# Optimization experiments

Measured on AMD Instinct MI355X. Metric: run time of the kernel, lower is better.

The kernel has to match this reference:

```python
import jax, jax.numpy as jnp
import numpy as np

EPS = 1e-5  # torch InstanceNorm1d default eps


def _instance_norm(x, gamma, beta):
    # per-sample, per-channel stats over the length dim; biased variance (torch semantics)
    mu = jnp.mean(x, axis=-1, keepdims=True)
    var = jnp.var(x, axis=-1, keepdims=True)
    return (x - mu) / jnp.sqrt(var + EPS) * gamma[None, :, None] + beta[None, :, None]


def _forward(x_ft, gamma, beta):
    # x_ft: complex [B, C, N]
    N = x_ft.shape[-1]
    x = jnp.real(jnp.fft.ifft(x_ft, norm='forward'))  # [B, C, N] real
    # The torch loop runs res = base_res .. N, each iteration overwriting the
    # low/high frequency bands of x_out in-place. The final iteration
    # (res == N) writes EVERY entry of x_out (the two band slices cover all
    # N//2+1 rfft bins), so the module's output -- and its gradients, since
    # overwritten writes carry zero cotangent -- equal the res == N
    # computation alone. resample_1d(x, N) copies the full spectrum and is a
    # spectral identity, so x_res == x.
    xr = _instance_norm(x, gamma, beta)
    xr = jax.nn.gelu(xr, approximate=False)  # exact GELU, matches torch nn.GELU
    # Faithful to the source: inside the loop torch.fft.rfft2 is used, i.e. a
    # 2D transform over the last two dims (channel, length).
    x_out = jnp.fft.rfft2(xr, norm='forward')  # complex [B, C, N//2 + 1]
    out = jnp.fft.fft(jnp.fft.irfft(x_out, n=N, norm='forward'), norm='forward')
    return out  # complex [B, C, N]


def setup_inputs() -> dict:
    key = jax.random.key(0)
    k1, k2 = jax.random.split(key)
    B, C, N = 16, 128, 8192
    return {
        'x_ft_real': jax.random.normal(k1, (B, C, N), dtype=jnp.float32),
        'x_ft_imag': jax.random.normal(k2, (B, C, N), dtype=jnp.float32),
        'gamma': jnp.ones((C,), dtype=jnp.float32),
        'beta': jnp.zeros((C,), dtype=jnp.float32),
    }


def reference(x_ft_real, x_ft_imag, gamma, beta):
    out = _forward(jax.lax.complex(x_ft_real, x_ft_imag), gamma, beta)
    # return real/imag parts as separate float arrays (harness-friendly)
    return (jnp.real(out), jnp.imag(out))
```

## Files before the change

kernel.cpp:

```cpp
#include <hip/hip_runtime.h>
#include <math.h>

static constexpr int kN = 8192;
static constexpr int kC = 128;
static constexpr int kB = 16;
static constexpr float kScale = 0.5f / 1048576.0f;

#define C8  0.70710678118654752f
#define CP8 0.92387953251128676f
#define SP8 0.38268343236508977f

typedef float v2f __attribute__((ext_vector_type(2)));

__device__ __forceinline__ v2f mk2(float x, float y){ v2f r; r.x=x; r.y=y; return r; }
__device__ __forceinline__ v2f imul(v2f a){ return mk2(-a.y, a.x); }
__device__ __forceinline__ v2f mimul(v2f a){ return mk2(a.y, -a.x); }
__device__ __forceinline__ v2f cconj(v2f a){ return mk2(a.x, -a.y); }
__device__ __forceinline__ v2f cmul(v2f a, v2f b){
    return mk2(a.x*b.x - a.y*b.y, a.x*b.y + a.y*b.x);
}

__device__ __forceinline__ v2f wrev(float rev){
    return mk2(__builtin_amdgcn_cosf(rev), __builtin_amdgcn_sinf(rev));
}

__device__ __forceinline__ int swz(int n){ return n ^ ((n>>4)&15); }

#define REV(k) ((((k)&3)<<2)|((k)>>2))

template<int SGN>
__device__ __forceinline__ void dft4(v2f&a, v2f&b, v2f&c, v2f&d){
    v2f t0=a+c, t1=a-c, t2=b+d, t3=b-d;
    v2f j3 = (SGN>0) ? imul(t3) : mimul(t3);
    a = t0+t2; b = t1+j3; c = t0-t2; d = t1-j3;
}

template<int SGN>
__device__ __forceinline__ void dft16(v2f* v){
    dft4<SGN>(v[0], v[4], v[8],  v[12]);
    dft4<SGN>(v[1], v[5], v[9],  v[13]);
    dft4<SGN>(v[2], v[6], v[10], v[14]);
    dft4<SGN>(v[3], v[7], v[11], v[15]);
    const float sg = (SGN>0)? 1.f : -1.f;
    const v2f W1 = mk2(CP8,  sg*SP8);
    const v2f W2 = mk2(C8,   sg*C8);
    const v2f W3 = mk2(SP8,  sg*CP8);
    const v2f W6 = mk2(-C8,  sg*C8);
    const v2f W9 = mk2(-CP8, -sg*SP8);
    v[5]  = cmul(v[5],  W1);
    v[9]  = cmul(v[9],  W2);
    v[13] = cmul(v[13], W3);
    v[6]  = cmul(v[6],  W2);
    v[10] = (SGN>0)? imul(v[10]) : mimul(v[10]);
    v[14] = cmul(v[14], W6);
    v[7]  = cmul(v[7],  W3);
    v[11] = cmul(v[11], W6);
    v[15] = cmul(v[15], W9);
    dft4<SGN>(v[0],  v[1],  v[2],  v[3]);
    dft4<SGN>(v[4],  v[5],  v[6],  v[7]);
    dft4<SGN>(v[8],  v[9],  v[10], v[11]);
    dft4<SGN>(v[12], v[13], v[14], v[15]);
}

__device__ __forceinline__ void twid_dif(v2f* v, v2f w1){
    v2f w2=cmul(w1,w1), w3=cmul(w2,w1), w4=cmul(w2,w2);
    v2f w5=cmul(w2,w3), w6=cmul(w3,w3), w7=cmul(w3,w4), w8=cmul(w4,w4);
    v2f w9=cmul(w4,w5), w10=cmul(w5,w5), w11=cmul(w5,w6), w12=cmul(w6,w6);
    v2f w13=cmul(w6,w7), w14=cmul(w7,w7), w15=cmul(w7,w8);
    v[4] =cmul(v[4], w1);  v[8] =cmul(v[8], w2);  v[12]=cmul(v[12],w3);
    v[1] =cmul(v[1], w4);  v[5] =cmul(v[5], w5);  v[9] =cmul(v[9], w6);
    v[13]=cmul(v[13],w7);  v[2] =cmul(v[2], w8);  v[6] =cmul(v[6], w9);
    v[10]=cmul(v[10],w10); v[14]=cmul(v[14],w11); v[3] =cmul(v[3], w12);
    v[7] =cmul(v[7], w13); v[11]=cmul(v[11],w14); v[15]=cmul(v[15],w15);
}
__device__ __forceinline__ void twid_dit(v2f* v, v2f w1){
    v2f w2=cmul(w1,w1), w3=cmul(w2,w1), w4=cmul(w2,w2);
    v2f w5=cmul(w2,w3), w6=cmul(w3,w3), w7=cmul(w3,w4), w8=cmul(w4,w4);
    v2f w9=cmul(w4,w5), w10=cmul(w5,w5), w11=cmul(w5,w6), w12=cmul(w6,w6);
    v2f w13=cmul(w6,w7), w14=cmul(w7,w7), w15=cmul(w7,w8);
    v[1] =cmul(v[1], w1);  v[2] =cmul(v[2], w2);  v[3] =cmul(v[3], w3);
    v[4] =cmul(v[4], w4);  v[5] =cmul(v[5], w5);  v[6] =cmul(v[6], w6);
    v[7] =cmul(v[7], w7);  v[8] =cmul(v[8], w8);  v[9] =cmul(v[9], w9);
    v[10]=cmul(v[10],w10); v[11]=cmul(v[11],w11); v[12]=cmul(v[12],w12);
    v[13]=cmul(v[13],w13); v[14]=cmul(v[14],w14); v[15]=cmul(v[15],w15);
}

__device__ __forceinline__ v2f gelu2(v2f v){
    v2f z = v * (0.7978845608028654f + 0.0356774081363001f * v * v);
    float e0 = __builtin_amdgcn_exp2f(-2.8853900817779268f * z.x);
    float e1 = __builtin_amdgcn_exp2f(-2.8853900817779268f * z.y);
    return mk2(v.x / (1.0f + e0), v.y / (1.0f + e1));
}

__global__ __launch_bounds__(256, 4) void k1_row(
    const float* __restrict__ xr, const float* __restrict__ xi,
    const float* __restrict__ gamma, const float* __restrict__ beta,
    float* __restrict__ outR, float* __restrict__ outI)
{
    __shared__ v2f buf[4096];
    __shared__ v2f Twb[16];
    __shared__ float sred[4];

    const int p   = threadIdx.x;
    const int row = blockIdx.x;
    const int ch  = row & (kC-1);

    if (p < 16) Twb[p] = wrev((float)p * (1.0f/256.0f));
    const int i0 = ((p>>4)<<8) + (p&15);

    v2f v[16];

    const float* rR = xr + (size_t)row * kN;
    const float* rI = xi + (size_t)row * kN;

    const float mean = 2.0f * rR[0];

    float pq = 0.f;
    #pragma unroll
    for (int j = 0; j < 16; ++j) {
        int k   = p + (j<<8);
        int km  = (kN - k) & (kN-1);
        int km2 = 4096 - k;
        v2f w = wrev((float)k * (1.0f/8192.0f));
        v2f Hk  = mk2(rR[k]+rR[km],       rI[k]-rI[km]);
        v2f Hk2 = mk2(rR[k+4096]+rR[km2], rI[k+4096]-rI[km2]);
        pq += Hk.x*Hk.x + Hk.y*Hk.y + Hk2.x*Hk2.x + Hk2.y*Hk2.y;
        v2f S = Hk + Hk2, D = Hk - Hk2;
        v2f P = cmul(D, w);
        v[j] = S + imul(P);
    }
    #pragma unroll
    for (int off = 32; off >= 1; off >>= 1)
        pq += __shfl_down(pq, off);
    if ((p & 63) == 0) sred[p>>6] = pq;

    dft16<1>(v);
    twid_dif(v, wrev((float)p * (1.0f/4096.0f)));
    #pragma unroll
    for (int m = 0; m < 16; ++m) buf[swz(p + (m<<8))] = v[REV(m)];
    __syncthreads();

    float total = sred[0] + sred[1] + sred[2] + sred[3];
    float var  = total - mean*mean;
    float gg = gamma[ch] * rsqrtf(var + 1e-5f);
    float bb = beta[ch] - mean * gg;

    const v2f wB = Twb[p & 15];
    #pragma unroll
    for (int j = 0; j < 16; ++j) v[j] = buf[swz(i0 + (j<<4))];
    dft16<1>(v);
    twid_dif(v, wB);
    #pragma unroll
    for (int m = 0; m < 16; ++m) buf[swz(i0 + (m<<4))] = v[REV(m)];
    __builtin_amdgcn_wave_barrier();

    #pragma unroll
    for (int j = 0; j < 16; ++j) v[j] = buf[swz((p<<4) + j)];
    dft16<1>(v);

    #pragma unroll
    for (int j = 0; j < 16; ++j) v[j] = gelu2(v[j] * gg + bb);

    {
        v2f u[16];
        #pragma unroll
        for (int j = 0; j < 16; ++j) u[j] = v[REV(j)];
        dft16<-1>(u);
        #pragma unroll
        for (int m = 0; m < 16; ++m) buf[swz((p<<4) + m)] = u[REV(m)];
    }
    __builtin_amdgcn_wave_barrier();

    #pragma unroll
    for (int j = 0; j < 16; ++j) v[j] = buf[swz(i0 + (j<<4))];
    twid_dit(v, cconj(wB));
    dft16<-1>(v);
    #pragma unroll
    for (int m = 0; m < 16; ++m) buf[swz(i0 + (m<<4))] = v[REV(m)];
    __syncthreads();

    #pragma unroll
    for (int j = 0; j < 16; ++j) v[j] = buf[swz(p + (j<<8))];
    twid_dit(v, cconj(wrev((float)p * (1.0f/4096.0f))));
    dft16<-1>(v);
    float* oR = outR + (size_t)row * kN;
    float* oI = outI + (size_t)row * kN;
    #pragma unroll
    for (int m = 0; m < 16; ++m) {
        int k = p + (m<<8);
        oR[k] = v[REV(m)].x;
        oI[k] = v[REV(m)].y;
    }
}

__global__ __launch_bounds__(256, 2) void k2_col(float* __restrict__ outR,
                                                 float* __restrict__ outI)
{
    __shared__ v2f tile[kC][32];
    __shared__ v2f tw[64];

    const int tid  = threadIdx.x;
    const int j    = tid & 31;
    const int g    = tid >> 5;
    const int b    = blockIdx.y;
    const int k0   = blockIdx.x << 5;
    const int colA = k0 + j;
    const bool valid = (colA <= 2048);
    const int colB = (4096 - colA) & 4095;

    if (tid < 64) {
        tw[tid] = mk2(__builtin_amdgcn_cosf((float)tid * (1.0f/128.0f)),
                      -__builtin_amdgcn_sinf((float)tid * (1.0f/128.0f)));
    }
    const float wc =  __builtin_amdgcn_cosf((float)colA * (1.0f/8192.0f));
    const float ws = -__builtin_amdgcn_sinf((float)colA * (1.0f/8192.0f));

    float* baseR = outR + (size_t)b * kC * kN;
    float* baseI = outI + (size_t)b * kC * kN;

    v2f yb[16];
    #pragma unroll
    for (int ci = 0; ci < 16; ++ci) {
        const int c = g + (ci << 3);
        v2f YA = mk2(0.f, 0.f), YB = mk2(0.f, 0.f);
        if (valid) {
            size_t offA = (size_t)c * kN + colA;
            size_t offB = (size_t)c * kN + colB;
            float Zx  = baseR[offA], Zy  = baseI[offA];
            float Zmx = baseR[offB], Zmy = baseI[offB];
            float Sx = Zx + Zmx, Sy = Zy - Zmy;
            float Dx = Zx - Zmx, Dy = Zy + Zmy;
            float Px = Dx*wc - Dy*ws, Py = Dx*ws + Dy*wc;
            YA = mk2(Sx + Py,  Sy - Px);
            YB = mk2(Sx - Py, -Sy - Px);
        }
        tile[c][j] = YA;
        yb[ci] = YB;
    }
    __syncthreads();

    for (int st = 7; st >= 1; --st) {
        const int h = 1 << (st-1);
        #pragma unroll
        for (int s = 0; s < 8; ++s) {
            int q   = g + (s<<3);
            int pos = q & (h-1);
            int i0  = ((q >> (st-1)) << st) + pos;
            int i1  = i0 + h;
            v2f a = tile[i0][j], bb = tile[i1][j];
            v2f w = tw[pos << (7-st)];
            tile[i0][j] = a + bb;
            tile[i1][j] = cmul(a - bb, w);
        }
        __syncthreads();
    }
    if (valid) {
        for (int p = g; p < kC; p += 8) {
            int f = (int)(__brev((unsigned)p) >> 25);
            v2f vv = tile[p][j] * kScale;
            size_t off = (size_t)f * kN + colA;
            if (colA == 0) {
                baseR[off] = vv.x; baseI[off] = 0.f;
            } else {
                baseR[off] = vv.x; baseI[off] = vv.y;
                size_t offm = (size_t)f * kN + (kN - colA);
                baseR[offm] = vv.x; baseI[offm] = -vv.y;
            }
        }
    }
    __syncthreads();

    #pragma unroll
    for (int ci = 0; ci < 16; ++ci) {
        const int c = g + (ci << 3);
        tile[c][j] = yb[ci];
    }
    __syncthreads();

    for (int st = 7; st >= 1; --st) {
        const int h = 1 << (st-1);
        #pragma unroll
        for (int s = 0; s < 8; ++s) {
            int q   = g + (s<<3);
            int pos = q & (h-1);
            int i0  = ((q >> (st-1)) << st) + pos;
            int i1  = i0 + h;
            v2f a = tile[i0][j], bb = tile[i1][j];
            v2f w = tw[pos << (7-st)];
            tile[i0][j] = a + bb;
            tile[i1][j] = cmul(a - bb, w);
        }
        __syncthreads();
    }
    if (valid) {
        const int kkB = 4096 - colA;
        for (int p = g; p < kC; p += 8) {
            int f = (int)(__brev((unsigned)p) >> 25);
            v2f vv = tile[p][j] * kScale;
            size_t off = (size_t)f * kN + kkB;
            if (kkB == 4096) {
                baseR[off] = vv.x; baseI[off] = 0.f;
            } else {
                baseR[off] = vv.x; baseI[off] = vv.y;
                size_t offm = (size_t)f * kN + (kN - kkB);
                baseR[offm] = vv.x; baseI[offm] = -vv.y;
            }
        }
    }
}

extern "C" void kernel_launch(void* const* d_in, const int* in_sizes, int n_in,
                              void* d_out, int out_size, void* d_ws, size_t ws_size,
                              hipStream_t stream)
{
    const float* xr    = (const float*)d_in[0];
    const float* xi    = (const float*)d_in[1];
    const float* gamma = (const float*)d_in[2];
    const float* beta  = (const float*)d_in[3];

    float* outR = (float*)d_out;
    float* outI = outR + (size_t)kB * kC * kN;

    k1_row<<<kB * kC, 256, 0, stream>>>(xr, xi, gamma, beta, outR, outI);
    k2_col<<<dim3(65, kB), 256, 0, stream>>>(outR, outI);
}
```

Before: 107.8 us.

## Process two rows per block in row FFT kernel with float4 LDS packing

The row kernel now handles two rows per 256-thread block, interleaving both rows' FFT stages so twiddle computation, barriers and LDS traffic are shared, with float4 shared-memory accesses carrying both rows. The bit-reverse copy before the inverse DFT16 is replaced by a dft16_rev variant that takes natural-order input. The goal is to amortise per-row fixed costs and raise instruction-level parallelism. In exchange, register pressure roughly doubles, launch bounds drop to 2 blocks per CU, shared memory doubles to 64KB, and the grid halves to 1024 blocks.

After: 117.9 us. +9.4%, slower.

```diff
diff --git a/kernel.cpp b/kernel.cpp
--- a/kernel.cpp
+++ b/kernel.cpp
@@ -62,27 +62,74 @@
     dft4<SGN>(v[12], v[13], v[14], v[15]);
 }
 
-__device__ __forceinline__ void twid_dif(v2f* v, v2f w1){
+template<int SGN>
+__device__ __forceinline__ void dft16_rev(v2f* v){
+    dft4<SGN>(v[0],  v[1],  v[2],  v[3]);
+    dft4<SGN>(v[4],  v[5],  v[6],  v[7]);
+    dft4<SGN>(v[8],  v[9],  v[10], v[11]);
+    dft4<SGN>(v[12], v[13], v[14], v[15]);
+    const float sg = (SGN>0)? 1.f : -1.f;
+    const v2f W1 = mk2(CP8,  sg*SP8);
+    const v2f W2 = mk2(C8,   sg*C8);
+    const v2f W3 = mk2(SP8,  sg*CP8);
+    const v2f W6 = mk2(-C8,  sg*C8);
+    const v2f W9 = mk2(-CP8, -sg*SP8);
+    v[5]  = cmul(v[5],  W1);
+    v[6]  = cmul(v[6],  W2);
+    v[7]  = cmul(v[7],  W3);
+    v[9]  = cmul(v[9],  W2);
+    v[10] = (SGN>0)? imul(v[10]) : mimul(v[10]);
+    v[11] = cmul(v[11], W6);
+    v[13] = cmul(v[13], W3);
+    v[14] = cmul(v[14], W6);
+    v[15] = cmul(v[15], W9);
+    dft4<SGN>(v[0], v[4], v[8],  v[12]);
+    dft4<SGN>(v[1], v[5], v[9],  v[13]);
+    dft4<SGN>(v[2], v[6], v[10], v[14]);
+    dft4<SGN>(v[3], v[7], v[11], v[15]);
+}
+
+__device__ __forceinline__ void twid_dif2(v2f* a, v2f* b, v2f w1){
     v2f w2=cmul(w1,w1), w3=cmul(w2,w1), w4=cmul(w2,w2);
     v2f w5=cmul(w2,w3), w6=cmul(w3,w3), w7=cmul(w3,w4), w8=cmul(w4,w4);
     v2f w9=cmul(w4,w5), w10=cmul(w5,w5), w11=cmul(w5,w6), w12=cmul(w6,w6);
     v2f w13=cmul(w6,w7), w14=cmul(w7,w7), w15=cmul(w7,w8);
-    v[4] =cmul(v[4], w1);  v[8] =cmul(v[8], w2);  v[12]=cmul(v[12],w3);
-    v[1] =cmul(v[1], w4);  v[5] =cmul(v[5], w5);  v[9] =cmul(v[9], w6);
-    v[13]=cmul(v[13],w7);  v[2] =cmul(v[2], w8);  v[6] =cmul(v[6], w9);
-    v[10]=cmul(v[10],w10); v[14]=cmul(v[14],w11); v[3] =cmul(v[3], w12);
-    v[7] =cmul(v[7], w13); v[11]=cmul(v[11],w14); v[15]=cmul(v[15],w15);
-}
-__device__ __forceinline__ void twid_dit(v2f* v, v2f w1){
+    a[4] =cmul(a[4], w1);  b[4] =cmul(b[4], w1);
+    a[8] =cmul(a[8], w2);  b[8] =cmul(b[8], w2);
+    a[12]=cmul(a[12],w3);  b[12]=cmul(b[12],w3);
+    a[1] =cmul(a[1], w4);  b[1] =cmul(b[1], w4);
+    a[5] =cmul(a[5], w5);  b[5] =cmul(b[5], w5);
+    a[9] =cmul(a[9], w6);  b[9] =cmul(b[9], w6);
+    a[13]=cmul(a[13],w7);  b[13]=cmul(b[13],w7);
+    a[2] =cmul(a[2], w8);  b[2] =cmul(b[2], w8);
+    a[6] =cmul(a[6], w9);  b[6] =cmul(b[6], w9);
+    a[10]=cmul(a[10],w10); b[10]=cmul(b[10],w10);
+    a[14]=cmul(a[14],w11); b[14]=cmul(b[14],w11);
+    a[3] =cmul(a[3], w12); b[3] =cmul(b[3], w12);
+    a[7] =cmul(a[7], w13); b[7] =cmul(b[7], w13);
+    a[11]=cmul(a[11],w14); b[11]=cmul(b[11],w14);
+    a[15]=cmul(a[15],w15); b[15]=cmul(b[15],w15);
+}
+__device__ __forceinline__ void twid_dit2(v2f* a, v2f* b, v2f w1){
     v2f w2=cmul(w1,w1), w3=cmul(w2,w1), w4=cmul(w2,w2);
     v2f w5=cmul(w2,w3), w6=cmul(w3,w3), w7=cmul(w3,w4), w8=cmul(w4,w4);
     v2f w9=cmul(w4,w5), w10=cmul(w5,w5), w11=cmul(w5,w6), w12=cmul(w6,w6);
     v2f w13=cmul(w6,w7), w14=cmul(w7,w7), w15=cmul(w7,w8);
-    v[1] =cmul(v[1], w1);  v[2] =cmul(v[2], w2);  v[3] =cmul(v[3], w3);
-    v[4] =cmul(v[4], w4);  v[5] =cmul(v[5], w5);  v[6] =cmul(v[6], w6);
-    v[7] =cmul(v[7], w7);  v[8] =cmul(v[8], w8);  v[9] =cmul(v[9], w9);
-    v[10]=cmul(v[10],w10); v[11]=cmul(v[11],w11); v[12]=cmul(v[12],w12);
-    v[13]=cmul(v[13],w13); v[14]=cmul(v[14],w14); v[15]=cmul(v[15],w15);
+    a[1] =cmul(a[1], w1);  b[1] =cmul(b[1], w1);
+    a[2] =cmul(a[2], w2);  b[2] =cmul(b[2], w2);
+    a[3] =cmul(a[3], w3);  b[3] =cmul(b[3], w3);
+    a[4] =cmul(a[4], w4);  b[4] =cmul(b[4], w4);
+    a[5] =cmul(a[5], w5);  b[5] =cmul(b[5], w5);
+    a[6] =cmul(a[6], w6);  b[6] =cmul(b[6], w6);
+    a[7] =cmul(a[7], w7);  b[7] =cmul(b[7], w7);
+    a[8] =cmul(a[8], w8);  b[8] =cmul(b[8], w8);
+    a[9] =cmul(a[9], w9);  b[9] =cmul(b[9], w9);
+    a[10]=cmul(a[10],w10); b[10]=cmul(b[10],w10);
+    a[11]=cmul(a[11],w11); b[11]=cmul(b[11],w11);
+    a[12]=cmul(a[12],w12); b[12]=cmul(b[12],w12);
+    a[13]=cmul(a[13],w13); b[13]=cmul(b[13],w13);
+    a[14]=cmul(a[14],w14); b[14]=cmul(b[14],w14);
+    a[15]=cmul(a[15],w15); b[15]=cmul(b[15],w15);
 }
 
 __device__ __forceinline__ v2f gelu2(v2f v){
@@ -92,104 +139,141 @@
     return mk2(v.x / (1.0f + e0), v.y / (1.0f + e1));
 }
 
-__global__ __launch_bounds__(256, 4) void k1_row(
+__global__ __launch_bounds__(256, 2) void k1_row(
     const float* __restrict__ xr, const float* __restrict__ xi,
     const float* __restrict__ gamma, const float* __restrict__ beta,
     float* __restrict__ outR, float* __restrict__ outI)
 {
-    __shared__ v2f buf[4096];
+    __shared__ float4 buf[4096];
     __shared__ v2f Twb[16];
-    __shared__ float sred[4];
-
-    const int p   = threadIdx.x;
-    const int row = blockIdx.x;
-    const int ch  = row & (kC-1);
+    __shared__ v2f sred[4];
+
+    const int p    = threadIdx.x;
+    const int row0 = blockIdx.x * 2;
 
     if (p < 16) Twb[p] = wrev((float)p * (1.0f/256.0f));
     const int i0 = ((p>>4)<<8) + (p&15);
 
-    v2f v[16];
-
-    const float* rR = xr + (size_t)row * kN;
-    const float* rI = xi + (size_t)row * kN;
-
-    const float mean = 2.0f * rR[0];
-
-    float pq = 0.f;
+    v2f v0[16], v1[16];
+
+    const float* r0R = xr + (size_t)row0 * kN;
+    const float* r0I = xi + (size_t)row0 * kN;
+    const float* r1R = r0R + kN;
+    const float* r1I = r0I + kN;
+
+    const float mean0 = 2.0f * r0R[0];
+    const float mean1 = 2.0f * r1R[0];
+
+    float pq0 = 0.f, pq1 = 0.f;
     #pragma unroll
     for (int j = 0; j < 16; ++j) {
         int k   = p + (j<<8);
         int km  = (kN - k) & (kN-1);
         int km2 = 4096 - k;
         v2f w = wrev((float)k * (1.0f/8192.0f));
-        v2f Hk  = mk2(rR[k]+rR[km],       rI[k]-rI[km]);
-        v2f Hk2 = mk2(rR[k+4096]+rR[km2], rI[k+4096]-rI[km2]);
-        pq += Hk.x*Hk.x + Hk.y*Hk.y + Hk2.x*Hk2.x + Hk2.y*Hk2.y;
-        v2f S = Hk + Hk2, D = Hk - Hk2;
-        v2f P = cmul(D, w);
-        v[j] = S + imul(P);
-    }
-    #pragma unroll
-    for (int off = 32; off >= 1; off >>= 1)
-        pq += __shfl_down(pq, off);
-    if ((p & 63) == 0) sred[p>>6] = pq;
-
-    dft16<1>(v);
-    twid_dif(v, wrev((float)p * (1.0f/4096.0f)));
-    #pragma unroll
-    for (int m = 0; m < 16; ++m) buf[swz(p + (m<<8))] = v[REV(m)];
+        {
+            v2f Hk  = mk2(r0R[k]+r0R[km],       r0I[k]-r0I[km]);
+            v2f Hk2 = mk2(r0R[k+4096]+r0R[km2], r0I[k+4096]-r0I[km2]);
+            pq0 += Hk.x*Hk.x + Hk.y*Hk.y + Hk2.x*Hk2.x + Hk2.y*Hk2.y;
+            v2f S = Hk + Hk2, D = Hk - Hk2;
+            v2f P = cmul(D, w);
+            v0[j] = S + imul(P);
+        }
+        {
+            v2f Hk  = mk2(r1R[k]+r1R[km],       r1I[k]-r1I[km]);
+            v2f Hk2 = mk2(r1R[k+4096]+r1R[km2], r1I[k+4096]-r1I[km2]);
+            pq1 += Hk.x*Hk.x + Hk.y*Hk.y + Hk2.x*Hk2.x + Hk2.y*Hk2.y;
+            v2f S = Hk + Hk2, D = Hk - Hk2;
+            v2f P = cmul(D, w);
+            v1[j] = S + imul(P);
+        }
+    }
+    #pragma unroll
+    for (int off = 32; off >= 1; off >>= 1) {
+        pq0 += __shfl_down(pq0, off);
+        pq1 += __shfl_down(pq1, off);
+    }
+    if ((p & 63) == 0) sred[p>>6] = mk2(pq0, pq1);
+
+    dft16<1>(v0); dft16<1>(v1);
+    twid_dif2(v0, v1, wrev((float)p * (1.0f/4096.0f)));
+    #pragma unroll
+    for (int m = 0; m < 16; ++m)
+        buf[swz(p + (m<<8))] = make_float4(v0[REV(m)].x, v0[REV(m)].y,
+                                           v1[REV(m)].x, v1[REV(m)].y);
     __syncthreads();
 
-    float total = sred[0] + sred[1] + sred[2] + sred[3];
-    float var  = total - mean*mean;
-    float gg = gamma[ch] * rsqrtf(var + 1e-5f);
-    float bb = beta[ch] - mean * gg;
+    v2f q0 = sred[0], q1 = sred[1], q2 = sred[2], q3 = sred[3];
+    float t0 = q0.x + q1.x + q2.x + q3.x;
+    float t1 = q0.y + q1.y + q2.y + q3.y;
+    const int ch0 = row0 & (kC-1), ch1 = (row0+1) & (kC-1);
+    float gg0 = gamma[ch0] * rsqrtf(t0 - mean0*mean0 + 1e-5f);
+    float bb0 = beta[ch0] - mean0 * gg0;
+    float gg1 = gamma[ch1] * rsqrtf(t1 - mean1*mean1 + 1e-5f);
+    float bb1 = beta[ch1] - mean1 * gg1;
 
     const v2f wB = Twb[p & 15];
     #pragma unroll
-    for (int j = 0; j < 16; ++j) v[j] = buf[swz(i0 + (j<<4))];
-    dft16<1>(v);
-    twid_dif(v, wB);
-    #pragma unroll
-    for (int m = 0; m < 16; ++m) buf[swz(i0 + (m<<4))] = v[REV(m)];
+    for (int j = 0; j < 16; ++j) {
+        float4 p4 = buf[swz(i0 + (j<<4))];
+        v0[j] = mk2(p4.x, p4.y); v1[j] = mk2(p4.z, p4.w);
+    }
+    dft16<1>(v0); dft16<1>(v1);
+    twid_dif2(v0, v1, wB);
+    #pragma unroll
+    for (int m = 0; m < 16; ++m)
+        buf[swz(i0 + (m<<4))] = make_float4(v0[REV(m)].x, v0[REV(m)].y,
+                                            v1[REV(m)].x, v1[REV(m)].y);
     __builtin_amdgcn_wave_barrier();
 
     #pragma unroll
-    for (int j = 0; j < 16; ++j) v[j] = buf[swz((p<<4) + j)];
-    dft16<1>(v);
-
-    #pragma unroll
-    for (int j = 0; j < 16; ++j) v[j] = gelu2(v[j] * gg + bb);
-
-    {
-        v2f u[16];
-        #pragma unroll
-        for (int j = 0; j < 16; ++j) u[j] = v[REV(j)];
-        dft16<-1>(u);
-        #pragma unroll
-        for (int m = 0; m < 16; ++m) buf[swz((p<<4) + m)] = u[REV(m)];
-    }
+    for (int j = 0; j < 16; ++j) {
+        float4 p4 = buf[swz((p<<4) + j)];
+        v0[j] = mk2(p4.x, p4.y); v1[j] = mk2(p4.z, p4.w);
+    }
+    dft16<1>(v0); dft16<1>(v1);
+
+    #pragma unroll
+    for (int j = 0; j < 16; ++j) {
+        v0[j] = gelu2(v0[j] * gg0 + bb0);
+        v1[j] = gelu2(v1[j] * gg1 + bb1);
+    }
+
+    dft16_rev<-1>(v0); dft16_rev<-1>(v1);
+    #pragma unroll
+    for (int m = 0; m < 16; ++m)
+        buf[swz((p<<4) + m)] = make_float4(v0[m].x, v0[m].y, v1[m].x, v1[m].y);
     __builtin_amdgcn_wave_barrier();
 
     #pragma unroll
-    for (int j = 0; j < 16; ++j) v[j] = buf[swz(i0 + (j<<4))];
-    twid_dit(v, cconj(wB));
-    dft16<-1>(v);
-    #pragma unroll
-    for (int m = 0; m < 16; ++m) buf[swz(i0 + (m<<4))] = v[REV(m)];
+    for (int j = 0; j < 16; ++j) {
+        float4 p4 = buf[swz(i0 + (j<<4))];
+        v0[j] = mk2(p4.x, p4.y); v1[j] = mk2(p4.z, p4.w);
+    }
+    twid_dit2(v0, v1, cconj(wB));
+    dft16<-1>(v0); dft16<-1>(v1);
+    #pragma unroll
+    for (int m = 0; m < 16; ++m)
+        buf[swz(i0 + (m<<4))] = make_float4(v0[REV(m)].x, v0[REV(m)].y,
+                                            v1[REV(m)].x, v1[REV(m)].y);
     __syncthreads();
 
     #pragma unroll
-    for (int j = 0; j < 16; ++j) v[j] = buf[swz(p + (j<<8))];
-    twid_dit(v, cconj(wrev((float)p * (1.0f/4096.0f))));
-    dft16<-1>(v);
-    float* oR = outR + (size_t)row * kN;
-    float* oI = outI + (size_t)row * kN;
+    for (int j = 0; j < 16; ++j) {
+        float4 p4 = buf[swz(p + (j<<8))];
+        v0[j] = mk2(p4.x, p4.y); v1[j] = mk2(p4.z, p4.w);
+    }
+    twid_dit2(v0, v1, cconj(wrev((float)p * (1.0f/4096.0f))));
+    dft16<-1>(v0); dft16<-1>(v1);
+    float* o0R = outR + (size_t)row0 * kN;
+    float* o0I = outI + (size_t)row0 * kN;
+    float* o1R = o0R + kN;
+    float* o1I = o0I + kN;
     #pragma unroll
     for (int m = 0; m < 16; ++m) {
         int k = p + (m<<8);
-        oR[k] = v[REV(m)].x;
-        oI[k] = v[REV(m)].y;
+        o0R[k] = v0[REV(m)].x;  o0I[k] = v0[REV(m)].y;
+        o1R[k] = v1[REV(m)].x;  o1I[k] = v1[REV(m)].y;
     }
 }
 
@@ -321,6 +405,6 @@
     float* outR = (float*)d_out;
     float* outI = outR + (size_t)kB * kC * kN;
 
-    k1_row<<<kB * kC, 256, 0, stream>>>(xr, xi, gamma, beta, outR, outI);
+    k1_row<<<kB * kC / 2, 256, 0, stream>>>(xr, xi, gamma, beta, outR, outI);
     k2_col<<<dim3(65, kB), 256, 0, stream>>>(outR, outI);
 }
```
